# Optimization experiments

Measured on AMD Instinct MI355X. Metric: run time of the kernel, lower is better.

The kernel has to match this reference:

```python
import jax, jax.numpy as jnp
import numpy as np

N_FFT = 8192  # config.n (next power of two of 2*seq_len)


def setup_inputs() -> dict:
    key = jax.random.key(0)
    k1, k2, k3, k4 = jax.random.split(key, 4)
    x = jax.random.normal(k1, (2, 4096, 128), dtype=jnp.float32)
    spectral_filters = jax.random.normal(k2, (4096, 16), dtype=jnp.float32)
    # nn.Parameter tensors (zeros in torch init; randomized for a meaningful test)
    M_phi_plus = jax.random.normal(k3, (16, 128, 128), dtype=jnp.float32) * 0.02
    M_phi_minus = jax.random.normal(k4, (16, 128, 128), dtype=jnp.float32) * 0.02
    return {
        "x": x,
        "spectral_filters": spectral_filters,
        "M_phi_plus": M_phi_plus,
        "M_phi_minus": M_phi_minus,
    }


def reference(x, spectral_filters, M_phi_plus, M_phi_minus):
    # STU forward, use_tensordot=False, use_hankel_L=False.
    B, L, D = x.shape
    K = spectral_filters.shape[1]
    n = N_FFT

    # sgn[l] = (-1)^l : the "negative featurization" sign flip
    sgn = jnp.where(jnp.arange(L) % 2 == 0, 1.0, -1.0).astype(x.dtype)  # (L,)

    # FFT of the K spectral filters: (F, K), F = n//2 + 1
    Vf = jnp.fft.rfft(spectral_filters, n=n, axis=0)

    # FFTs of u and sign-flipped u (convolution is linear, so we avoid the
    # torch expand to (B, L, K, D) before the FFT): (B, F, D)
    Uf_plus = jnp.fft.rfft(x, n=n, axis=1)
    Uf_minus = jnp.fft.rfft(x * sgn[None, :, None], n=n, axis=1)

    # Pointwise multiply in frequency, broadcast over K and D: (B, F, K, D)
    U_plus = jnp.fft.irfft(Vf[None, :, :, None] * Uf_plus[:, :, None, :], n=n, axis=1)[:, :L]
    U_minus = jnp.fft.irfft(Vf[None, :, :, None] * Uf_minus[:, :, None, :], n=n, axis=1)[:, :L]
    U_minus = U_minus * sgn[None, :, None, None]  # undo sign on outputs

    # Contract (B, L, K, D) with (K, D, D_out)  ==  reshape(B,L,K*D) @ (K*D, D_out)
    spectral_plus = jnp.einsum("blkd,kde->ble", U_plus, M_phi_plus)
    spectral_minus = jnp.einsum("blkd,kde->ble", U_minus, M_phi_minus)
    return spectral_plus + spectral_minus
```

## Files before the change

kernel.cpp:

```cpp
#include <hip/hip_runtime.h>
#include <stdint.h>

#define N2   8192
#define N    4096
#define LOGN 12
#define F_TOT 4097
#define FP    4112
#define D    128
#define K    16
#define B    2
#define PI_F 3.14159265358979323846f
#define NPAD (N + (N >> 5))

typedef _Float16 f16x8 __attribute__((ext_vector_type(8)));
typedef float    f32x4 __attribute__((ext_vector_type(4)));
typedef float    f32x2v __attribute__((ext_vector_type(2)));

__device__ __forceinline__ void gload_lds16(const void* g, void* l) {
  __builtin_amdgcn_global_load_lds((const __attribute__((address_space(1))) uint32_t*)g,
                                   (__attribute__((address_space(3))) uint32_t*)l, 16, 0, 0);
}

__device__ __forceinline__ int pad(int w) { return w + (w >> 5); }

__device__ __forceinline__ _Float16 hpick(uint32_t w, int hi) {
  union { unsigned short u; _Float16 h; } c;
  c.u = (unsigned short)(hi ? (w >> 16) : (w & 0xffffu));
  return c.h;
}

__device__ __forceinline__ uint32_t packh2(float a, float b) {
  union { uint32_t u; unsigned short s[2]; } p;
  union { unsigned short u; _Float16 h; } ca, cb;
  ca.h = (_Float16)a; cb.h = (_Float16)b;
  p.s[0] = ca.u; p.s[1] = cb.u;
  return p.u;
}

__device__ __forceinline__ float2 ntload2(const float2* p) {
  f32x2v v = __builtin_nontemporal_load((const f32x2v*)p);
  return make_float2(v.x, v.y);
}

__device__ __forceinline__ void fill_tw(float2* tw, int tid, int nthr) {
  for (int i = tid + 1; i < N; i += nthr) {
    int s = 31 - __clz(i);
    int j = i - (1 << s);
    float ang = PI_F * (float)j / (float)(1 << s);
    float wi_, wr_; __sincosf(ang, &wi_, &wr_);
    tw[i] = make_float2(wr_, wi_);
  }
}

__device__ __forceinline__ void fft_lds(float* re, float* im, const float2* tw,
                                        int tid, int nthr, float sign) {
  for (int s = 0; s < LOGN; s += 2) {
    const int len = 1 << s;
    for (int t = tid; t < (N >> 2); t += nthr) {
      const int j = t & (len - 1);
      const int base = ((t >> s) << (s + 2)) + j;
      const int i0 = pad(base), i1 = pad(base + len);
      const int i2 = pad(base + 2 * len), i3 = pad(base + 3 * len);
      float2 w1 = tw[len + j];
      float2 w2 = tw[2 * len + j];
      float2 w3 = tw[3 * len + j];
      const float w1r = w1.x, w1i = sign * w1.y;
      const float w2r = w2.x, w2i = sign * w2.y;
      const float w3r = w3.x, w3i = sign * w3.y;
      float x0r = re[i0], x0i = im[i0];
      float x1r = re[i1], x1i = im[i1];
      float x2r = re[i2], x2i = im[i2];
      float x3r = re[i3], x3i = im[i3];
      float t1r = w1r * x1r - w1i * x1i, t1i = w1r * x1i + w1i * x1r;
      float t3r = w1r * x3r - w1i * x3i, t3i = w1r * x3i + w1i * x3r;
      float b0r = x0r + t1r, b0i = x0i + t1i;
      float b1r = x0r - t1r, b1i = x0i - t1i;
      float b2r = x2r + t3r, b2i = x2i + t3i;
      float b3r = x2r - t3r, b3i = x2i - t3i;
      float u2r = w2r * b2r - w2i * b2i, u2i = w2r * b2i + w2i * b2r;
      float u3r = w3r * b3r - w3i * b3i, u3i = w3r * b3i + w3i * b3r;
      re[i0] = b0r + u2r; im[i0] = b0i + u2i;
      re[i2] = b0r - u2r; im[i2] = b0i - u2i;
      re[i1] = b1r + u3r; im[i1] = b1i + u3i;
      re[i3] = b1r - u3r; im[i3] = b1i - u3i;
    }
    __syncthreads();
  }
}

__global__ __launch_bounds__(256) void transpose_x(const float* __restrict__ x,
                                                   float* __restrict__ xT) {
  __shared__ float t[32][33];
  const int b = blockIdx.z;
  const int l0 = blockIdx.x * 32, d0 = blockIdx.y * 32;
  const int c = threadIdx.x & 31, r0 = threadIdx.x >> 5;
#pragma unroll
  for (int i = 0; i < 4; ++i) {
    int r = r0 + i * 8;
    t[r][c] = x[((size_t)b * N + l0 + r) * D + d0 + c];
  }
  __syncthreads();
#pragma unroll
  for (int i = 0; i < 4; ++i) {
    int r = r0 + i * 8;
    xT[((size_t)b * D + d0 + r) * N + l0 + c] = t[c][r];
  }
}

__global__ __launch_bounds__(256) void transpose_out(const float* __restrict__ outT,
                                                     float* __restrict__ out) {
  __shared__ float t[32][33];
  const int b = blockIdx.z;
  const int l0 = blockIdx.x * 32, d0 = blockIdx.y * 32;
  const int c = threadIdx.x & 31, r0 = threadIdx.x >> 5;
#pragma unroll
  for (int i = 0; i < 4; ++i) {
    int r = r0 + i * 8;
    t[r][c] = outT[((size_t)b * D + d0 + r) * N + l0 + c];
  }
  __syncthreads();
#pragma unroll
  for (int i = 0; i < 4; ++i) {
    int r = r0 + i * 8;
    __builtin_nontemporal_store(t[c][r], &out[((size_t)b * N + l0 + r) * D + d0 + c]);
  }
}

__global__ __launch_bounds__(1024) void fwd_fft(const float* __restrict__ xT,
                                                const float* __restrict__ filt,
                                                const float* __restrict__ Mp,
                                                const float* __restrict__ Mm,
                                                uint32_t* __restrict__ Ufh,
                                                float2* __restrict__ Vf,
                                                _Float16* __restrict__ Mt) {
  __shared__ float re[NPAD];
  __shared__ float im[NPAD];
  __shared__ float2 tw[N];
  const int tid = threadIdx.x;
  const int sig = blockIdx.x;

  if (sig >= B * D + K) {
    const int pid = sig - (B * D + K);
    const int k = pid & 15, h = pid >> 4;
    const float* src = (h ? Mm : Mp) + (size_t)k * D * D;
    for (int d0 = 0; d0 < D; d0 += 16) {
      for (int i = tid; i < 16 * D; i += 1024) re[i] = src[(size_t)d0 * D + i];
      __syncthreads();
      if (tid < 256) {
        const int e = tid >> 1, c0 = (tid & 1) * 8;
        f16x8 w;
#pragma unroll
        for (int j = 0; j < 8; ++j) w[j] = (_Float16)re[(c0 + j) * D + e];
        const int eq = e >> 5, el = e & 31;
        const size_t kd8 = (size_t)(d0 + c0) >> 3;
        *(f16x8*)(Mt + (((((size_t)h * 4 + eq) * K + k) * 16 + kd8) * 32 + el) * 8) = w;
      }
      __syncthreads();
    }
    return;
  }

  fill_tw(tw, tid, 1024);

  const float* in; int istride;
  int b = 0, d = 0, k = 0;
  const bool isx = sig < B * D;
  if (isx) { b = sig >> 7; d = sig & (D - 1); in = xT + ((size_t)b * D + d) * N; istride = 1; }
  else     { k = sig - B * D; in = filt + k; istride = K; }

  for (int m = tid; m < N; m += 1024) {
    float vr = 0.f, vi = 0.f;
    if (m < (N >> 1)) {
      if (istride == 1) { float2 z = ((const float2*)in)[m]; vr = z.x; vi = z.y; }
      else { vr = in[(size_t)(2 * m) * istride]; vi = in[(size_t)(2 * m + 1) * istride]; }
    }
    int dst = pad(__brev(m) >> (32 - LOGN));
    re[dst] = vr; im[dst] = vi;
  }
  __syncthreads();
  fft_lds(re, im, tw, tid, 1024, -1.0f);

  for (int f = tid; f <= (N >> 1); f += 1024) {
    int f2 = f & (N - 1), fn = (N - f) & (N - 1);
    float zr = re[pad(f2)], zi = im[pad(f2)];
    float nr = re[pad(fn)], ni = im[pad(fn)];
    float Er = 0.5f * (zr + nr), Ei = 0.5f * (zi - ni);
    float Or = 0.5f * (zi + ni), Oi = -0.5f * (zr - nr);
    float ang = -PI_F * (float)f / (float)N;
    float wi_, wr_; __sincosf(ang, &wi_, &wr_);
    float X0r = Er + wr_ * Or - wi_ * Oi;
    float X0i = Ei + wr_ * Oi + wi_ * Or;
    float X1r = Er - wr_ * Or + wi_ * Oi;
    float X1i = -Ei + wr_ * Oi + wi_ * Or;
    if (isx) {
      uint32_t* o = Ufh + ((size_t)b * F_TOT) * D + d;
      o[(size_t)f * D]       = packh2(X0r, X0i);
      o[(size_t)(N - f) * D] = packh2(X1r, X1i);
    } else {
      Vf[(size_t)f * K + k]       = make_float2(X0r, X0i);
      Vf[(size_t)(N - f) * K + k] = make_float2(X1r, X1i);
    }
  }
}

__global__ __launch_bounds__(256, 3) void middle_mfma(const uint32_t* __restrict__ Ufh,
                                                      const float2* __restrict__ Vf,
                                                      const _Float16* __restrict__ Mt,
                                                      float2* __restrict__ Gt) {
  __shared__ __align__(16) char smem[8192 + 2 * 16384];
  float2*   Vl   = (float2*)smem;
  char*     bbuf = smem + 8192;

  const int tid = threadIdx.x;
  const int l = tid & 63, w = tid >> 6;
  const int l15 = l & 15, g = l >> 4;
  const int fg = w >> 1, eg = w & 1;
  const int eq = blockIdx.y, ks = blockIdx.z;
  const int fx = blockIdx.x * 32;
  const int fo = l15 >> 2, bb = (l15 >> 1) & 1, ri = l15 & 1;

  auto STAGE = [&](int buf, int kk) {
    const int kg = ks * 8 + kk;
#pragma unroll
    for (int i = 0; i < 4; ++i) {
      const int oe = w * 2048 + i * 512;
      const int pm = oe >> 12, within = oe & 4095;
      const _Float16* src = Mt + (((size_t)pm * 4 + eq) * K + kg) * 4096 + within + l * 8;
      gload_lds16((const void*)src,
                  (void*)(bbuf + (size_t)buf * 16384 + (size_t)oe * 2));
    }
  };
  STAGE(0, 0);

  {
    const int fl = tid >> 3, kq = tid & 7;
    int fe = fx + fl; if (fe > N) fe = N;
    *(float4*)&Vl[((size_t)0 * 32 + fl) * 16 + kq * 2] =
        *(const float4*)&Vf[(size_t)fe * K + kq * 2];
    *(float4*)&Vl[((size_t)1 * 32 + fl) * 16 + kq * 2] =
        *(const float4*)&Vf[(size_t)(N - fe) * K + kq * 2];
  }

  f16x8 A[4][4];
#pragma unroll
  for (int s = 0; s < 4; ++s) {
    int f = fx + fg * 16 + s * 4 + fo; if (f > N) f = N;
    const uint4* ur = (const uint4*)(Ufh + ((size_t)bb * F_TOT + f) * D);
#pragma unroll
    for (int ds = 0; ds < 4; ++ds) {
      uint4 w0 = ur[ds * 8 + g * 2];
      uint4 w1 = ur[ds * 8 + g * 2 + 1];
      f16x8 a;
      a[0] = hpick(w0.x, ri); a[1] = hpick(w0.y, ri);
      a[2] = hpick(w0.z, ri); a[3] = hpick(w0.w, ri);
      a[4] = hpick(w1.x, ri); a[5] = hpick(w1.y, ri);
      a[6] = hpick(w1.z, ri); a[7] = hpick(w1.w, ri);
      A[s][ds] = a;
    }
  }

  f32x4 acc[4];
#pragma unroll
  for (int s = 0; s < 4; ++s) acc[s] = (f32x4)0.f;

  asm volatile("s_waitcnt vmcnt(0)" ::: "memory");
  __syncthreads();

  int buf = 0;
  for (int st = 0; st < 8; ++st) {
    if (st < 7) STAGE(buf ^ 1, st + 1);
    const int kg = ks * 8 + st;
    const _Float16* bc = (const _Float16*)(bbuf + (size_t)buf * 16384);

#pragma unroll
    for (int pm = 0; pm < 2; ++pm) {
      float2 vv[4];
#pragma unroll
      for (int s = 0; s < 4; ++s)
        vv[s] = Vl[((size_t)pm * 32 + fg * 16 + s * 4 + g) * 16 + kg];

      f32x4 P[4];
#pragma unroll
      for (int ds = 0; ds < 4; ++ds) {
        f16x8 bf = *(const f16x8*)(bc + (size_t)pm * 4096 +
                                   (size_t)((ds * 4 + g) * 32 + eg * 16 + l15) * 8);
#pragma unroll
        for (int s = 0; s < 4; ++s) {
          f32x4 cin = (ds == 0) ? (f32x4)0.f : P[s];
          P[s] = __builtin_amdgcn_mfma_f32_16x16x32_f16(A[s][ds], bf, cin, 0, 0, 0);
        }
      }
#pragma unroll
      for (int s = 0; s < 4; ++s) {
        const float vr = vv[s].x, vy = vv[s].y;
        if (pm == 0) {
          acc[s][0] += vr * P[s][0] - vy * P[s][1];
          acc[s][1] += vy * P[s][0] + vr * P[s][1];
          acc[s][2] += vr * P[s][2] - vy * P[s][3];
          acc[s][3] += vy * P[s][2] + vr * P[s][3];
        } else {
          acc[s][0] += vr * P[s][0] + vy * P[s][1];
          acc[s][1] += vr * P[s][1] - vy * P[s][0];
          acc[s][2] += vr * P[s][2] + vy * P[s][3];
          acc[s][3] += vr * P[s][3] - vy * P[s][2];
        }
      }
    }
    asm volatile("s_waitcnt vmcnt(0)" ::: "memory");
    __syncthreads();
    buf ^= 1;
  }

  float2* tr = (float2*)smem;
#pragma unroll
  for (int s = 0; s < 4; ++s) {
    const int fl = fg * 16 + s * 4 + g;
    const int el = eg * 16 + l15;
    tr[(size_t)el * 33 + fl]        = make_float2(acc[s][0], acc[s][1]);
    tr[(size_t)(32 + el) * 33 + fl] = make_float2(acc[s][2], acc[s][3]);
  }
  __syncthreads();
  const size_t slab = (size_t)ks * B * D * FP;
#pragma unroll
  for (int p = 0; p < 4; ++p) {
    const int row = p * 16 + (tid >> 4);
    const int bo = row >> 5, e_gl = eq * 32 + (row & 31);
    const int c = (tid & 15) * 2;
    const int fgl = fx + c;
    if (fgl < F_TOT) {
      float2 v0 = tr[(size_t)row * 33 + c], v1 = tr[(size_t)row * 33 + c + 1];
      f32x4 v = {v0.x, v0.y, v1.x, v1.y};
      __builtin_nontemporal_store(v, (f32x4*)&Gt[slab + ((size_t)bo * D + e_gl) * FP + fgl]);
    }
  }
}

__global__ __launch_bounds__(1024) void inv_fft(const float2* __restrict__ Gt,
                                                float* __restrict__ outT) {
  __shared__ float re[NPAD];
  __shared__ float im[NPAD];
  __shared__ float2 tw[N];
  const int tid = threadIdx.x;
  const int sig = blockIdx.x;
  const int b = sig >> 7, e = sig & (D - 1);
  const float2* g0 = Gt + ((size_t)b * D + e) * FP;
  const size_t pstr = (size_t)B * D * FP;

  fill_tw(tw, tid, 1024);

  for (int kk = tid; kk <= (N >> 1); kk += 1024) {
    float2 a0 = ntload2(&g0[kk]);
    float2 a1 = ntload2(&g0[pstr + kk]);
    float2 b0 = ntload2(&g0[N - kk]);
    float2 b1 = ntload2(&g0[pstr + (N - kk)]);
    float Xkx = a0.x + a1.x, Xky = a0.y + a1.y;
    float Xnx = b0.x + b1.x, Xny = b0.y + b1.y;
    float Er = 0.5f * (Xkx + Xnx), Ei = 0.5f * (Xky - Xny);
    float Dr = 0.5f * (Xkx - Xnx), Di = 0.5f * (Xky + Xny);
    float ang = PI_F * (float)kk / (float)N;
    float wi_, wr_; __sincosf(ang, &wi_, &wr_);
    float Or = Dr * wr_ - Di * wi_;
    float Oi = Dr * wi_ + Di * wr_;
    int d1 = pad(__brev(kk) >> (32 - LOGN));
    re[d1] = Er - Oi; im[d1] = Ei + Or;
    if (kk != 0 && kk != (N >> 1)) {
      int d2 = pad(__brev(N - kk) >> (32 - LOGN));
      re[d2] = Er + Oi; im[d2] = -Ei + Or;
    }
  }
  __syncthreads();
  fft_lds(re, im, tw, tid, 1024, +1.0f);
  const float scale = 1.0f / (float)N;
  float2* ob = (float2*)(outT + ((size_t)b * D + e) * N);
  for (int m = tid; m < (N >> 1); m += 1024) {
    int i0 = pad(m);
    ob[m] = make_float2(re[i0] * scale, im[i0] * scale);
  }
}

extern "C" void kernel_launch(void* const* d_in, const int* in_sizes, int n_in,
                              void* d_out, int out_size, void* d_ws, size_t ws_size,
                              hipStream_t stream) {
  const float* x  = (const float*)d_in[0];
  const float* fl = (const float*)d_in[1];
  const float* Mp = (const float*)d_in[2];
  const float* Mm = (const float*)d_in[3];
  float* out = (float*)d_out;

  float*    xT  = (float*)d_ws;
  uint32_t* Ufh = (uint32_t*)(xT + (size_t)B * D * N);
  float2*   Vf  = (float2*)(Ufh + (size_t)B * F_TOT * D);
  float2*   Gt  = Vf + (size_t)F_TOT * K;
  _Float16* Mt  = (_Float16*)(Gt + (size_t)2 * B * D * FP);

  transpose_x<<<dim3(N / 32, D / 32, B), 256, 0, stream>>>(x, xT);
  fwd_fft<<<B * D + K + 32, 1024, 0, stream>>>(xT, fl, Mp, Mm, Ufh, Vf, Mt);
  middle_mfma<<<dim3(129, 4, 2), 256, 0, stream>>>(Ufh, Vf, Mt, Gt);
  inv_fft<<<B * D, 1024, 0, stream>>>(Gt, xT);
  transpose_out<<<dim3(N / 32, D / 32, B), 256, 0, stream>>>(xT, out);
}
```

Before: 70.32 us.

## Drop K-split in middle MFMA, loop all K per block and remap grid

The middle kernel no longer splits the K filter dimension across two slabs. Each block now iterates over all 16 filters and writes one Gt slab, so inv_fft reads half the data and skips the partial-sum add. The grid becomes a 1-D launch of 544 blocks with a swizzle that groups 8 consecutive frequency tiles per eq. Surplus blocks exit early. This halves the block count and doubles per-block serial work, which may reduce occupancy and parallelism in exchange for less global traffic.

```diff
diff --git a/kernel.cpp b/kernel.cpp
--- a/kernel.cpp
+++ b/kernel.cpp
@@ -211,21 +211,25 @@
   float2*   Vl   = (float2*)smem;
   char*     bbuf = smem + 8192;
 
+  const int lin = blockIdx.x;
+  const int r8 = lin & 7, m = lin >> 3;
+  const int fx8 = (m >> 2) * 8 + r8;
+  const int eq  = m & 3;
+  if (fx8 > 128) return;
+  const int fx = fx8 * 32;
+
   const int tid = threadIdx.x;
   const int l = tid & 63, w = tid >> 6;
   const int l15 = l & 15, g = l >> 4;
   const int fg = w >> 1, eg = w & 1;
-  const int eq = blockIdx.y, ks = blockIdx.z;
-  const int fx = blockIdx.x * 32;
   const int fo = l15 >> 2, bb = (l15 >> 1) & 1, ri = l15 & 1;
 
   auto STAGE = [&](int buf, int kk) {
-    const int kg = ks * 8 + kk;
 #pragma unroll
     for (int i = 0; i < 4; ++i) {
       const int oe = w * 2048 + i * 512;
       const int pm = oe >> 12, within = oe & 4095;
-      const _Float16* src = Mt + (((size_t)pm * 4 + eq) * K + kg) * 4096 + within + l * 8;
+      const _Float16* src = Mt + (((size_t)pm * 4 + eq) * K + kk) * 4096 + within + l * 8;
       gload_lds16((const void*)src,
                   (void*)(bbuf + (size_t)buf * 16384 + (size_t)oe * 2));
     }
@@ -267,9 +271,8 @@
   __syncthreads();
 
   int buf = 0;
-  for (int st = 0; st < 8; ++st) {
-    if (st < 7) STAGE(buf ^ 1, st + 1);
-    const int kg = ks * 8 + st;
+  for (int st = 0; st < K; ++st) {
+    if (st < K - 1) STAGE(buf ^ 1, st + 1);
     const _Float16* bc = (const _Float16*)(bbuf + (size_t)buf * 16384);
 
 #pragma unroll
@@ -277,7 +280,7 @@
       float2 vv[4];
 #pragma unroll
       for (int s = 0; s < 4; ++s)
-        vv[s] = Vl[((size_t)pm * 32 + fg * 16 + s * 4 + g) * 16 + kg];
+        vv[s] = Vl[((size_t)pm * 32 + fg * 16 + s * 4 + g) * 16 + st];
 
       f32x4 P[4];
 #pragma unroll
@@ -320,7 +323,6 @@
     tr[(size_t)(32 + el) * 33 + fl] = make_float2(acc[s][2], acc[s][3]);
   }
   __syncthreads();
-  const size_t slab = (size_t)ks * B * D * FP;
 #pragma unroll
   for (int p = 0; p < 4; ++p) {
     const int row = p * 16 + (tid >> 4);
@@ -330,7 +332,7 @@
     if (fgl < F_TOT) {
       float2 v0 = tr[(size_t)row * 33 + c], v1 = tr[(size_t)row * 33 + c + 1];
       f32x4 v = {v0.x, v0.y, v1.x, v1.y};
-      __builtin_nontemporal_store(v, (f32x4*)&Gt[slab + ((size_t)bo * D + e_gl) * FP + fgl]);
+      __builtin_nontemporal_store(v, (f32x4*)&Gt[((size_t)bo * D + e_gl) * FP + fgl]);
     }
   }
 }
@@ -344,19 +346,14 @@
   const int sig = blockIdx.x;
   const int b = sig >> 7, e = sig & (D - 1);
   const float2* g0 = Gt + ((size_t)b * D + e) * FP;
-  const size_t pstr = (size_t)B * D * FP;
 
   fill_tw(tw, tid, 1024);
 
   for (int kk = tid; kk <= (N >> 1); kk += 1024) {
-    float2 a0 = ntload2(&g0[kk]);
-    float2 a1 = ntload2(&g0[pstr + kk]);
-    float2 b0 = ntload2(&g0[N - kk]);
-    float2 b1 = ntload2(&g0[pstr + (N - kk)]);
-    float Xkx = a0.x + a1.x, Xky = a0.y + a1.y;
-    float Xnx = b0.x + b1.x, Xny = b0.y + b1.y;
-    float Er = 0.5f * (Xkx + Xnx), Ei = 0.5f * (Xky - Xny);
-    float Dr = 0.5f * (Xkx - Xnx), Di = 0.5f * (Xky + Xny);
+    float2 Xk = ntload2(&g0[kk]);
+    float2 Xn = ntload2(&g0[N - kk]);
+    float Er = 0.5f * (Xk.x + Xn.x), Ei = 0.5f * (Xk.y - Xn.y);
+    float Dr = 0.5f * (Xk.x - Xn.x), Di = 0.5f * (Xk.y + Xn.y);
     float ang = PI_F * (float)kk / (float)N;
     float wi_, wr_; __sincosf(ang, &wi_, &wr_);
     float Or = Dr * wr_ - Di * wi_;
@@ -391,11 +388,11 @@
   uint32_t* Ufh = (uint32_t*)(xT + (size_t)B * D * N);
   float2*   Vf  = (float2*)(Ufh + (size_t)B * F_TOT * D);
   float2*   Gt  = Vf + (size_t)F_TOT * K;
-  _Float16* Mt  = (_Float16*)(Gt + (size_t)2 * B * D * FP);
+  _Float16* Mt  = (_Float16*)(Gt + (size_t)B * D * FP);
 
   transpose_x<<<dim3(N / 32, D / 32, B), 256, 0, stream>>>(x, xT);
   fwd_fft<<<B * D + K + 32, 1024, 0, stream>>>(xT, fl, Mp, Mm, Ufh, Vf, Mt);
-  middle_mfma<<<dim3(129, 4, 2), 256, 0, stream>>>(Ufh, Vf, Mt, Gt);
+  middle_mfma<<<544, 256, 0, stream>>>(Ufh, Vf, Mt, Gt);
   inv_fft<<<B * D, 1024, 0, stream>>>(Gt, xT);
   transpose_out<<<dim3(N / 32, D / 32, B), 256, 0, stream>>>(xT, out);
 }
```

After: 69.35 us, median of 3. Within noise of the previous version (-1.4%).
